# Kernel tuning notes

Hardware: AMD Instinct MI355X
Metric: run time of the kernel (lower is better)

Reference implementation:

```python
import jax, jax.numpy as jnp
import numpy as np

RANK_WEIGHT = 0.1  # init kwarg rank_weight
EPS = 1e-08


def setup_inputs() -> dict:
    key = jax.random.key(0)
    k1, k2, k3, k4 = jax.random.split(key, 4)
    B, D = 8192, 128
    return {
        "q_embeddings": jax.random.normal(k1, (B, D), dtype=jnp.float32),
        "a_embeddings": jax.random.normal(k2, (B, D), dtype=jnp.float32),
        "question_ids": jax.random.randint(k3, (B,), 0, 2048, dtype=jnp.int64),
        "ranks": jax.random.uniform(k4, (B,), dtype=jnp.float32),
    }


def reference(q_embeddings, a_embeddings, question_ids, ranks):
    # NOTE: the original computes q@a.T/temperature into `similarity` but the
    # per-sample loop recomputes sims WITHOUT temperature; we match the loop math.
    sims = jnp.matmul(q_embeddings, a_embeddings.T)  # [B, B]
    same_q = question_ids[:, None] == question_ids[None, :]  # [B, B] bool
    # pos_mask weight per positive column j: 1 - rank_weight * ranks[j]
    w = jnp.where(same_q, 1.0 - RANK_WEIGHT * ranks[None, :], 0.0)  # [B, B]
    # stable exp-ratio: sum(w*exp(s)) / sum(exp(s))
    m = jnp.max(sims, axis=1, keepdims=True)
    e = jnp.exp(sims - m)
    num = jnp.sum(w * e, axis=1)
    den = jnp.sum(e, axis=1)
    loss = jnp.mean(-jnp.log(num / den + EPS))
    pred = jnp.argmax(sims, axis=1)  # [B]
    correct = jnp.take_along_axis(w, pred[:, None], axis=1)[:, 0] > 0
    accuracy = jnp.mean(correct.astype(jnp.float32))
    return loss, accuracy
```

## Files before the change

### kernel.cpp

```cpp
#include <hip/hip_runtime.h>
#include <hip/hip_bf16.h>
#include <cmath>

#define B_N 8192
#define D_K 128
#define ROWS 64
#define CSPLIT 8
#define T_OUT 16

typedef short bf16x8 __attribute__((ext_vector_type(8)));
typedef unsigned short u16x8 __attribute__((ext_vector_type(8)));
typedef float f32x4  __attribute__((ext_vector_type(4)));

typedef __attribute__((address_space(3))) unsigned int as3_uint;
typedef __attribute__((address_space(1))) unsigned int as1_uint;

__device__ __forceinline__ void gl_lds16(const void* g, void* l) {
    __builtin_amdgcn_global_load_lds((const as1_uint*)(uintptr_t)g,
                                     (as3_uint*)(unsigned int)(uintptr_t)l,
                                     16, 0, 0);
}

__device__ inline unsigned short f2bf(float f) {
    unsigned u = __builtin_bit_cast(unsigned, f);
    u += 0x7fffu + ((u >> 16) & 1u);
    return (unsigned short)(u >> 16);
}

__global__ void cvt_kernel(const float* __restrict__ q, const float* __restrict__ a,
                           unsigned short* __restrict__ qb, unsigned short* __restrict__ ab,
                           float* __restrict__ out) {
    int g = blockIdx.x * blockDim.x + threadIdx.x;
    if (g < 2) out[g] = 0.0f;
    float4 q0 = reinterpret_cast<const float4*>(q)[g * 2];
    float4 q1 = reinterpret_cast<const float4*>(q)[g * 2 + 1];
    u16x8 oq;
    oq[0] = f2bf(q0.x); oq[1] = f2bf(q0.y); oq[2] = f2bf(q0.z); oq[3] = f2bf(q0.w);
    oq[4] = f2bf(q1.x); oq[5] = f2bf(q1.y); oq[6] = f2bf(q1.z); oq[7] = f2bf(q1.w);
    *reinterpret_cast<u16x8*>(qb + (size_t)g * 8) = oq;

    float4 a0 = reinterpret_cast<const float4*>(a)[g * 2];
    float4 a1 = reinterpret_cast<const float4*>(a)[g * 2 + 1];
    u16x8 oa;
    oa[0] = f2bf(a0.x); oa[1] = f2bf(a0.y); oa[2] = f2bf(a0.z); oa[3] = f2bf(a0.w);
    oa[4] = f2bf(a1.x); oa[5] = f2bf(a1.y); oa[6] = f2bf(a1.z); oa[7] = f2bf(a1.w);
    const int col = g >> 4, sq = g & 15, s = sq >> 2, quad = sq & 3;
    const int chunk = ((col >> 4) * 4 + s) * 64 + quad * 16 + (col & 15);
    *reinterpret_cast<u16x8*>(ab + (size_t)chunk * 8) = oa;
}

__launch_bounds__(256, 4)
__global__ void mpl_part_kernel(const unsigned short* __restrict__ qb,
                                const unsigned short* __restrict__ ab,
                                const int* __restrict__ qids,
                                const float* __restrict__ ranks,
                                float* __restrict__ pden, float* __restrict__ pnum,
                                float* __restrict__ pmax, float* __restrict__ pmaxp) {
    __shared__ unsigned short smem[2 * 8192];

    const int tid  = threadIdx.x;
    const int lane = tid & 63;
    const int wave = tid >> 6;
    const int rg   = blockIdx.x >> 3;
    const int cs   = blockIdx.x & 7;
    const int rowBase = rg * ROWS;
    const int quad = lane >> 4;
    const int l15  = lane & 15;

    bf16x8 qfrag[4];
    {
        const unsigned short* qrow = qb + (size_t)(rowBase + wave * 16 + l15) * D_K + quad * 8;
        #pragma unroll
        for (int s = 0; s < 4; ++s)
            qfrag[s] = *reinterpret_cast<const bf16x8*>(qrow + s * 32);
    }

    int qidrow[4];
    #pragma unroll
    for (int r = 0; r < 4; ++r)
        qidrow[r] = qids[rowBase + wave * 16 + quad * 4 + r];

    float den[4], num[4], mxv[4], mxp[4];
    #pragma unroll
    for (int r = 0; r < 4; ++r) {
        den[r] = 0.f; num[r] = 0.f; mxv[r] = -INFINITY; mxp[r] = -INFINITY;
    }

    const float L2E = 1.4426950408889634f;
    const float CB  = 64.0f;
    const int colStart = cs * 1024;

    const char* gstrip = (const char*)ab + (size_t)cs * 64 * 4096;
    const int   chunk  = (wave * 4) * 1024;

    #pragma unroll
    for (int r = 0; r < 4; ++r)
        gl_lds16(gstrip + chunk + r * 1024 + lane * 16,
                 (char*)smem + chunk + r * 1024);
    __syncthreads();

    for (int t = 0; t < T_OUT; ++t) {
        const int cur = t & 1, nxt = cur ^ 1;
        if (t + 1 < T_OUT) {
            const char* gsrc = gstrip + (size_t)(t + 1) * 16384 + chunk;
            char*       ldst = (char*)smem + nxt * 16384 + chunk;
            #pragma unroll
            for (int r = 0; r < 4; ++r)
                gl_lds16(gsrc + r * 1024 + lane * 16, ldst + r * 1024);
        }

        const unsigned short* lbase = smem + cur * 8192 + lane * 8;
        f32x4 acc[4];
        #pragma unroll
        for (int u = 0; u < 4; ++u) acc[u] = f32x4{0.f, 0.f, 0.f, 0.f};
        #pragma unroll
        for (int u = 0; u < 4; ++u)
            #pragma unroll
            for (int s = 0; s < 4; ++s) {
                bf16x8 bfrag = *reinterpret_cast<const bf16x8*>(lbase + u * 2048 + s * 512);
                acc[u] = __builtin_amdgcn_mfma_f32_16x16x32_bf16(qfrag[s], bfrag, acc[u], 0, 0, 0);
            }

        #pragma unroll
        for (int u = 0; u < 4; ++u) {
            const int c  = colStart + t * 64 + u * 16 + l15;
            const int qc = qids[c];
            const float wc = 1.0f - 0.1f * ranks[c];
            #pragma unroll
            for (int r = 0; r < 4; ++r) {
                float sv = acc[u][r];
                float e  = __builtin_amdgcn_exp2f(fmaf(sv, L2E, -CB));
                bool pos = (qc == qidrow[r]);
                den[r] += e;
                num[r] = fmaf(pos ? wc : 0.0f, e, num[r]);
                mxv[r] = fmaxf(mxv[r], sv);
                mxp[r] = fmaxf(mxp[r], pos ? sv : -INFINITY);
            }
        }
        __syncthreads();
    }

    #pragma unroll
    for (int m = 1; m <= 8; m <<= 1) {
        #pragma unroll
        for (int r = 0; r < 4; ++r) {
            den[r] += __shfl_xor(den[r], m, 64);
            num[r] += __shfl_xor(num[r], m, 64);
            mxv[r]  = fmaxf(mxv[r], __shfl_xor(mxv[r], m, 64));
            mxp[r]  = fmaxf(mxp[r], __shfl_xor(mxp[r], m, 64));
        }
    }

    if (l15 == 0) {
        const int rb = cs * B_N + rowBase + wave * 16 + quad * 4;
        #pragma unroll
        for (int r = 0; r < 4; ++r) {
            pden[rb + r]  = den[r];
            pnum[rb + r]  = num[r];
            pmax[rb + r]  = mxv[r];
            pmaxp[rb + r] = mxp[r];
        }
    }
}

__launch_bounds__(256, 4)
__global__ void fin_kernel(const float* __restrict__ pden, const float* __restrict__ pnum,
                           const float* __restrict__ pmax, const float* __restrict__ pmaxp,
                           float* __restrict__ out) {
    const int r = blockIdx.x * 256 + threadIdx.x;
    float d = 0.f, n = 0.f, mv = -INFINITY, mp = -INFINITY;
    #pragma unroll
    for (int cs = 0; cs < CSPLIT; ++cs) {
        d += pden[cs * B_N + r];
        n += pnum[cs * B_N + r];
        mv = fmaxf(mv, pmax[cs * B_N + r]);
        mp = fmaxf(mp, pmaxp[cs * B_N + r]);
    }
    float lsum = -logf(n / d + 1e-8f);
    float csum = (mp == mv) ? 1.0f : 0.0f;
    #pragma unroll
    for (int m = 1; m <= 32; m <<= 1) {
        lsum += __shfl_xor(lsum, m, 64);
        csum += __shfl_xor(csum, m, 64);
    }
    __shared__ float sl[4], sc[4];
    const int wave = threadIdx.x >> 6;
    if ((threadIdx.x & 63) == 0) { sl[wave] = lsum; sc[wave] = csum; }
    __syncthreads();
    if (threadIdx.x == 0) {
        float L = sl[0] + sl[1] + sl[2] + sl[3];
        float C = sc[0] + sc[1] + sc[2] + sc[3];
        atomicAdd(&out[0], L * (1.0f / B_N));
        atomicAdd(&out[1], C * (1.0f / B_N));
    }
}

extern "C" void kernel_launch(void* const* d_in, const int* in_sizes, int n_in,
                              void* d_out, int out_size, void* d_ws, size_t ws_size,
                              hipStream_t stream) {
    const float* q     = (const float*)d_in[0];
    const float* a     = (const float*)d_in[1];
    const int*   qids  = (const int*)d_in[2];
    const float* ranks = (const float*)d_in[3];
    float* out = (float*)d_out;

    unsigned short* qb = (unsigned short*)d_ws;
    unsigned short* ab = qb + (size_t)B_N * D_K;
    char* p = (char*)(ab + (size_t)B_N * D_K);
    float* pden  = (float*)p;                p += CSPLIT * B_N * sizeof(float);
    float* pnum  = (float*)p;                p += CSPLIT * B_N * sizeof(float);
    float* pmax  = (float*)p;                p += CSPLIT * B_N * sizeof(float);
    float* pmaxp = (float*)p;

    cvt_kernel<<<(B_N * D_K / 8) / 256, 256, 0, stream>>>(q, a, qb, ab, out);
    mpl_part_kernel<<<(B_N / ROWS) * CSPLIT, 256, 0, stream>>>(qb, ab, qids, ranks,
                                                               pden, pnum, pmax, pmaxp);
    fin_kernel<<<B_N / 256, 256, 0, stream>>>(pden, pnum, pmax, pmaxp, out);
}
```

Measured before the change: 99.82 us.

## Switch to 32x32x16 MFMA tiles with 256-row, 512-thread blocks

Replaces the 16x16x32 bf16 MFMA with the 32x32x16 variant, so each wave computes a 32x32 tile. The A-matrix pre-layout is rewritten to match the new B-fragment lane mapping. Blocks now cover 256 rows with 8 waves (512 threads), so each LDS-staged column tile is reused by four times as many rows, cutting global/LDS traffic per MFMA. In exchange, per-thread accumulator and reduction state grows to 16 rows, which raises register pressure and halves blocks per CU. The grid shrinks to 256 blocks, which may underfill the GPU.

```diff
diff --git a/kernel.cpp b/kernel.cpp
--- a/kernel.cpp
+++ b/kernel.cpp
@@ -4,13 +4,13 @@
 
 #define B_N 8192
 #define D_K 128
-#define ROWS 64
+#define ROWS 256
 #define CSPLIT 8
 #define T_OUT 16
 
 typedef short bf16x8 __attribute__((ext_vector_type(8)));
 typedef unsigned short u16x8 __attribute__((ext_vector_type(8)));
-typedef float f32x4  __attribute__((ext_vector_type(4)));
+typedef float f32x16 __attribute__((ext_vector_type(16)));
 
 typedef __attribute__((address_space(3))) unsigned int as3_uint;
 typedef __attribute__((address_space(1))) unsigned int as1_uint;
@@ -44,12 +44,14 @@
     u16x8 oa;
     oa[0] = f2bf(a0.x); oa[1] = f2bf(a0.y); oa[2] = f2bf(a0.z); oa[3] = f2bf(a0.w);
     oa[4] = f2bf(a1.x); oa[5] = f2bf(a1.y); oa[6] = f2bf(a1.z); oa[7] = f2bf(a1.w);
-    const int col = g >> 4, sq = g & 15, s = sq >> 2, quad = sq & 3;
-    const int chunk = ((col >> 4) * 4 + s) * 64 + quad * 16 + (col & 15);
-    *reinterpret_cast<u16x8*>(ab + (size_t)chunk * 8) = oa;
-}
-
-__launch_bounds__(256, 4)
+    const int col = g >> 4, sq = g & 15;
+    const int N = col >> 5, nl = col & 31;
+    const int s16 = sq >> 1, h = sq & 1;
+    const int lane = h * 32 + nl;
+    *reinterpret_cast<u16x8*>(ab + (size_t)(N * 8 + s16) * 512 + lane * 8) = oa;
+}
+
+__launch_bounds__(512, 2)
 __global__ void mpl_part_kernel(const unsigned short* __restrict__ qb,
                                 const unsigned short* __restrict__ ab,
                                 const int* __restrict__ qids,
@@ -63,26 +65,26 @@
     const int wave = tid >> 6;
     const int rg   = blockIdx.x >> 3;
     const int cs   = blockIdx.x & 7;
-    const int rowBase = rg * ROWS;
-    const int quad = lane >> 4;
-    const int l15  = lane & 15;
-
-    bf16x8 qfrag[4];
+    const int waveRow = rg * ROWS + wave * 32;
+    const int half = lane >> 5;
+    const int l31  = lane & 31;
+
+    bf16x8 qfrag[8];
     {
-        const unsigned short* qrow = qb + (size_t)(rowBase + wave * 16 + l15) * D_K + quad * 8;
-        #pragma unroll
-        for (int s = 0; s < 4; ++s)
-            qfrag[s] = *reinterpret_cast<const bf16x8*>(qrow + s * 32);
-    }
-
-    int qidrow[4];
-    #pragma unroll
-    for (int r = 0; r < 4; ++r)
-        qidrow[r] = qids[rowBase + wave * 16 + quad * 4 + r];
-
-    float den[4], num[4], mxv[4], mxp[4];
-    #pragma unroll
-    for (int r = 0; r < 4; ++r) {
+        const unsigned short* qrow = qb + (size_t)(waveRow + l31) * D_K + half * 8;
+        #pragma unroll
+        for (int s = 0; s < 8; ++s)
+            qfrag[s] = *reinterpret_cast<const bf16x8*>(qrow + s * 16);
+    }
+
+    int qidrow[16];
+    #pragma unroll
+    for (int r = 0; r < 16; ++r)
+        qidrow[r] = qids[waveRow + (r & 3) + 8 * (r >> 2) + 4 * half];
+
+    float den[16], num[16], mxv[16], mxp[16];
+    #pragma unroll
+    for (int r = 0; r < 16; ++r) {
         den[r] = 0.f; num[r] = 0.f; mxv[r] = -INFINITY; mxp[r] = -INFINITY;
     }
 
@@ -90,13 +92,13 @@
     const float CB  = 64.0f;
     const int colStart = cs * 1024;
 
-    const char* gstrip = (const char*)ab + (size_t)cs * 64 * 4096;
-    const int   chunk  = (wave * 4) * 1024;
-
-    #pragma unroll
-    for (int r = 0; r < 4; ++r)
-        gl_lds16(gstrip + chunk + r * 1024 + lane * 16,
-                 (char*)smem + chunk + r * 1024);
+    const char* gstrip = (const char*)ab + (size_t)cs * 262144;
+    const int   chunk  = wave * 2048;
+
+    #pragma unroll
+    for (int i = 0; i < 2; ++i)
+        gl_lds16(gstrip + chunk + i * 1024 + lane * 16,
+                 (char*)smem + chunk + i * 1024);
     __syncthreads();
 
     for (int t = 0; t < T_OUT; ++t) {
@@ -105,30 +107,29 @@
             const char* gsrc = gstrip + (size_t)(t + 1) * 16384 + chunk;
             char*       ldst = (char*)smem + nxt * 16384 + chunk;
             #pragma unroll
-            for (int r = 0; r < 4; ++r)
-                gl_lds16(gsrc + r * 1024 + lane * 16, ldst + r * 1024);
+            for (int i = 0; i < 2; ++i)
+                gl_lds16(gsrc + i * 1024 + lane * 16, ldst + i * 1024);
         }
 
         const unsigned short* lbase = smem + cur * 8192 + lane * 8;
-        f32x4 acc[4];
-        #pragma unroll
-        for (int u = 0; u < 4; ++u) acc[u] = f32x4{0.f, 0.f, 0.f, 0.f};
-        #pragma unroll
-        for (int u = 0; u < 4; ++u)
-            #pragma unroll
-            for (int s = 0; s < 4; ++s) {
-                bf16x8 bfrag = *reinterpret_cast<const bf16x8*>(lbase + u * 2048 + s * 512);
-                acc[u] = __builtin_amdgcn_mfma_f32_16x16x32_bf16(qfrag[s], bfrag, acc[u], 0, 0, 0);
-            }
-
-        #pragma unroll
-        for (int u = 0; u < 4; ++u) {
-            const int c  = colStart + t * 64 + u * 16 + l15;
+        #pragma unroll
+        for (int nt = 0; nt < 2; ++nt) {
+            const int c  = colStart + t * 64 + nt * 32 + l31;
             const int qc = qids[c];
             const float wc = 1.0f - 0.1f * ranks[c];
-            #pragma unroll
-            for (int r = 0; r < 4; ++r) {
-                float sv = acc[u][r];
+
+            f32x16 acc;
+            #pragma unroll
+            for (int i = 0; i < 16; ++i) acc[i] = 0.f;
+            #pragma unroll
+            for (int s = 0; s < 8; ++s) {
+                bf16x8 bfrag = *reinterpret_cast<const bf16x8*>(lbase + nt * 4096 + s * 512);
+                acc = __builtin_amdgcn_mfma_f32_32x32x16_bf16(qfrag[s], bfrag, acc, 0, 0, 0);
+            }
+
+            #pragma unroll
+            for (int r = 0; r < 16; ++r) {
+                float sv = acc[r];
                 float e  = __builtin_amdgcn_exp2f(fmaf(sv, L2E, -CB));
                 bool pos = (qc == qidrow[r]);
                 den[r] += e;
@@ -141,9 +142,9 @@
     }
 
     #pragma unroll
-    for (int m = 1; m <= 8; m <<= 1) {
-        #pragma unroll
-        for (int r = 0; r < 4; ++r) {
+    for (int m = 1; m <= 16; m <<= 1) {
+        #pragma unroll
+        for (int r = 0; r < 16; ++r) {
             den[r] += __shfl_xor(den[r], m, 64);
             num[r] += __shfl_xor(num[r], m, 64);
             mxv[r]  = fmaxf(mxv[r], __shfl_xor(mxv[r], m, 64));
@@ -151,14 +152,14 @@
         }
     }
 
-    if (l15 == 0) {
-        const int rb = cs * B_N + rowBase + wave * 16 + quad * 4;
-        #pragma unroll
-        for (int r = 0; r < 4; ++r) {
-            pden[rb + r]  = den[r];
-            pnum[rb + r]  = num[r];
-            pmax[rb + r]  = mxv[r];
-            pmaxp[rb + r] = mxp[r];
+    if (l31 == 0) {
+        #pragma unroll
+        for (int r = 0; r < 16; ++r) {
+            const int row = waveRow + (r & 3) + 8 * (r >> 2) + 4 * half;
+            pden[cs * B_N + row]  = den[r];
+            pnum[cs * B_N + row]  = num[r];
+            pmax[cs * B_N + row]  = mxv[r];
+            pmaxp[cs * B_N + row] = mxp[r];
         }
     }
 }
@@ -213,7 +214,7 @@
     float* pmaxp = (float*)p;
 
     cvt_kernel<<<(B_N * D_K / 8) / 256, 256, 0, stream>>>(q, a, qb, ab, out);
-    mpl_part_kernel<<<(B_N / ROWS) * CSPLIT, 256, 0, stream>>>(qb, ab, qids, ranks,
+    mpl_part_kernel<<<(B_N / ROWS) * CSPLIT, 512, 0, stream>>>(qb, ab, qids, ranks,
                                                                pden, pnum, pmax, pmaxp);
     fin_kernel<<<B_N / 256, 256, 0, stream>>>(pden, pnum, pmax, pmaxp, out);
 }
```

Result: slower. 104.9 us (+5.1%).

## Switch similarity GEMM from bf16 to fp8 MFMA with repacked LDS layout

Applied to the files above, without the earlier changes.

Embeddings are now converted to fp8 (e4m3) instead of bf16, and the similarity matmul uses the fp8 16x16x32 MFMA. The column-tile layout is repacked so each pipeline stage covers 128 columns in 16 KB of LDS, halving the loop trip count. The aim is to halve operand bandwidth and raise MFMA throughput. fp8 precision loss can change argmax ties and the accuracy metric, and it adds loss error that may exceed tolerance.

```diff
diff --git a/kernel.cpp b/kernel.cpp
--- a/kernel.cpp
+++ b/kernel.cpp
@@ -1,16 +1,14 @@
 #include <hip/hip_runtime.h>
-#include <hip/hip_bf16.h>
 #include <cmath>
 
 #define B_N 8192
 #define D_K 128
 #define ROWS 64
 #define CSPLIT 8
-#define T_OUT 16
-
-typedef short bf16x8 __attribute__((ext_vector_type(8)));
-typedef unsigned short u16x8 __attribute__((ext_vector_type(8)));
-typedef float f32x4  __attribute__((ext_vector_type(4)));
+#define T_OUT 8
+
+typedef float f32x4 __attribute__((ext_vector_type(4)));
+typedef long  lx2   __attribute__((ext_vector_type(2)));
 
 typedef __attribute__((address_space(3))) unsigned int as3_uint;
 typedef __attribute__((address_space(1))) unsigned int as1_uint;
@@ -21,42 +19,44 @@
                                      16, 0, 0);
 }
 
-__device__ inline unsigned short f2bf(float f) {
-    unsigned u = __builtin_bit_cast(unsigned, f);
-    u += 0x7fffu + ((u >> 16) & 1u);
-    return (unsigned short)(u >> 16);
-}
-
 __global__ void cvt_kernel(const float* __restrict__ q, const float* __restrict__ a,
-                           unsigned short* __restrict__ qb, unsigned short* __restrict__ ab,
+                           unsigned char* __restrict__ qp, unsigned char* __restrict__ ap,
                            float* __restrict__ out) {
-    int g = blockIdx.x * blockDim.x + threadIdx.x;
+    const int g = blockIdx.x * blockDim.x + threadIdx.x;
     if (g < 2) out[g] = 0.0f;
+
     float4 q0 = reinterpret_cast<const float4*>(q)[g * 2];
     float4 q1 = reinterpret_cast<const float4*>(q)[g * 2 + 1];
-    u16x8 oq;
-    oq[0] = f2bf(q0.x); oq[1] = f2bf(q0.y); oq[2] = f2bf(q0.z); oq[3] = f2bf(q0.w);
-    oq[4] = f2bf(q1.x); oq[5] = f2bf(q1.y); oq[6] = f2bf(q1.z); oq[7] = f2bf(q1.w);
-    *reinterpret_cast<u16x8*>(qb + (size_t)g * 8) = oq;
-
     float4 a0 = reinterpret_cast<const float4*>(a)[g * 2];
     float4 a1 = reinterpret_cast<const float4*>(a)[g * 2 + 1];
-    u16x8 oa;
-    oa[0] = f2bf(a0.x); oa[1] = f2bf(a0.y); oa[2] = f2bf(a0.z); oa[3] = f2bf(a0.w);
-    oa[4] = f2bf(a1.x); oa[5] = f2bf(a1.y); oa[6] = f2bf(a1.z); oa[7] = f2bf(a1.w);
-    const int col = g >> 4, sq = g & 15, s = sq >> 2, quad = sq & 3;
-    const int chunk = ((col >> 4) * 4 + s) * 64 + quad * 16 + (col & 15);
-    *reinterpret_cast<u16x8*>(ab + (size_t)chunk * 8) = oa;
+
+    int qw0 = __builtin_amdgcn_cvt_pk_fp8_f32(q0.x, q0.y, 0, false);
+    qw0     = __builtin_amdgcn_cvt_pk_fp8_f32(q0.z, q0.w, qw0, true);
+    int qw1 = __builtin_amdgcn_cvt_pk_fp8_f32(q1.x, q1.y, 0, false);
+    qw1     = __builtin_amdgcn_cvt_pk_fp8_f32(q1.z, q1.w, qw1, true);
+    int aw0 = __builtin_amdgcn_cvt_pk_fp8_f32(a0.x, a0.y, 0, false);
+    aw0     = __builtin_amdgcn_cvt_pk_fp8_f32(a0.z, a0.w, aw0, true);
+    int aw1 = __builtin_amdgcn_cvt_pk_fp8_f32(a1.x, a1.y, 0, false);
+    aw1     = __builtin_amdgcn_cvt_pk_fp8_f32(a1.z, a1.w, aw1, true);
+
+    *reinterpret_cast<int2*>(qp + (size_t)g * 8) = make_int2(qw0, qw1);
+
+    const int col = g >> 4, sq = g & 15;
+    const int s = sq >> 2, quad = sq & 3;
+    const int T = col >> 4, e = col & 15;
+    const size_t off = (size_t)T * 2048 + (size_t)(s >> 1) * 1024
+                     + (size_t)(quad * 16 + e) * 16 + (size_t)(s & 1) * 8;
+    *reinterpret_cast<int2*>(ap + off) = make_int2(aw0, aw1);
 }
 
 __launch_bounds__(256, 4)
-__global__ void mpl_part_kernel(const unsigned short* __restrict__ qb,
-                                const unsigned short* __restrict__ ab,
+__global__ void mpl_part_kernel(const unsigned char* __restrict__ qp,
+                                const unsigned char* __restrict__ ap,
                                 const int* __restrict__ qids,
                                 const float* __restrict__ ranks,
                                 float* __restrict__ pden, float* __restrict__ pnum,
                                 float* __restrict__ pmax, float* __restrict__ pmaxp) {
-    __shared__ unsigned short smem[2 * 8192];
+    __shared__ unsigned char smem[2 * 16384];
 
     const int tid  = threadIdx.x;
     const int lane = tid & 63;
@@ -67,12 +67,12 @@
     const int quad = lane >> 4;
     const int l15  = lane & 15;
 
-    bf16x8 qfrag[4];
+    long qfrag[4];
     {
-        const unsigned short* qrow = qb + (size_t)(rowBase + wave * 16 + l15) * D_K + quad * 8;
+        const unsigned char* qrow = qp + (size_t)(rowBase + wave * 16 + l15) * D_K + quad * 8;
         #pragma unroll
         for (int s = 0; s < 4; ++s)
-            qfrag[s] = *reinterpret_cast<const bf16x8*>(qrow + s * 32);
+            qfrag[s] = *reinterpret_cast<const long*>(qrow + s * 32);
     }
 
     int qidrow[4];
@@ -90,13 +90,13 @@
     const float CB  = 64.0f;
     const int colStart = cs * 1024;
 
-    const char* gstrip = (const char*)ab + (size_t)cs * 64 * 4096;
-    const int   chunk  = (wave * 4) * 1024;
-
-    #pragma unroll
-    for (int r = 0; r < 4; ++r)
-        gl_lds16(gstrip + chunk + r * 1024 + lane * 16,
-                 (char*)smem + chunk + r * 1024);
+    const char* gstrip = (const char*)ap + (size_t)cs * 131072;
+    const int   chunk  = wave * 4096;
+
+    #pragma unroll
+    for (int i = 0; i < 4; ++i)
+        gl_lds16(gstrip + chunk + i * 1024 + lane * 16,
+                 (char*)smem + chunk + i * 1024);
     __syncthreads();
 
     for (int t = 0; t < T_OUT; ++t) {
@@ -105,30 +105,28 @@
             const char* gsrc = gstrip + (size_t)(t + 1) * 16384 + chunk;
             char*       ldst = (char*)smem + nxt * 16384 + chunk;
             #pragma unroll
-            for (int r = 0; r < 4; ++r)
-                gl_lds16(gsrc + r * 1024 + lane * 16, ldst + r * 1024);
-        }
-
-        const unsigned short* lbase = smem + cur * 8192 + lane * 8;
-        f32x4 acc[4];
-        #pragma unroll
-        for (int u = 0; u < 4; ++u) acc[u] = f32x4{0.f, 0.f, 0.f, 0.f};
-        #pragma unroll
-        for (int u = 0; u < 4; ++u)
-            #pragma unroll
-            for (int s = 0; s < 4; ++s) {
-                bf16x8 bfrag = *reinterpret_cast<const bf16x8*>(lbase + u * 2048 + s * 512);
-                acc[u] = __builtin_amdgcn_mfma_f32_16x16x32_bf16(qfrag[s], bfrag, acc[u], 0, 0, 0);
-            }
-
-        #pragma unroll
-        for (int u = 0; u < 4; ++u) {
-            const int c  = colStart + t * 64 + u * 16 + l15;
+            for (int i = 0; i < 4; ++i)
+                gl_lds16(gsrc + i * 1024 + lane * 16, ldst + i * 1024);
+        }
+
+        const unsigned char* lbase = smem + cur * 16384 + lane * 16;
+        #pragma unroll
+        for (int u = 0; u < 8; ++u) {
+            lx2 b01 = *reinterpret_cast<const lx2*>(lbase + u * 2048);
+            lx2 b23 = *reinterpret_cast<const lx2*>(lbase + u * 2048 + 1024);
+
+            f32x4 acc = {0.f, 0.f, 0.f, 0.f};
+            acc = __builtin_amdgcn_mfma_f32_16x16x32_fp8_fp8(qfrag[0], b01[0], acc, 0, 0, 0);
+            acc = __builtin_amdgcn_mfma_f32_16x16x32_fp8_fp8(qfrag[1], b01[1], acc, 0, 0, 0);
+            acc = __builtin_amdgcn_mfma_f32_16x16x32_fp8_fp8(qfrag[2], b23[0], acc, 0, 0, 0);
+            acc = __builtin_amdgcn_mfma_f32_16x16x32_fp8_fp8(qfrag[3], b23[1], acc, 0, 0, 0);
+
+            const int c  = colStart + t * 128 + u * 16 + l15;
             const int qc = qids[c];
             const float wc = 1.0f - 0.1f * ranks[c];
             #pragma unroll
             for (int r = 0; r < 4; ++r) {
-                float sv = acc[u][r];
+                float sv = acc[r];
                 float e  = __builtin_amdgcn_exp2f(fmaf(sv, L2E, -CB));
                 bool pos = (qc == qidrow[r]);
                 den[r] += e;
@@ -204,16 +202,16 @@
     const float* ranks = (const float*)d_in[3];
     float* out = (float*)d_out;
 
-    unsigned short* qb = (unsigned short*)d_ws;
-    unsigned short* ab = qb + (size_t)B_N * D_K;
-    char* p = (char*)(ab + (size_t)B_N * D_K);
+    unsigned char* qp = (unsigned char*)d_ws;
+    unsigned char* ap = qp + (size_t)B_N * D_K;
+    char* p = (char*)(ap + (size_t)B_N * D_K);
     float* pden  = (float*)p;                p += CSPLIT * B_N * sizeof(float);
     float* pnum  = (float*)p;                p += CSPLIT * B_N * sizeof(float);
     float* pmax  = (float*)p;                p += CSPLIT * B_N * sizeof(float);
     float* pmaxp = (float*)p;
 
-    cvt_kernel<<<(B_N * D_K / 8) / 256, 256, 0, stream>>>(q, a, qb, ab, out);
-    mpl_part_kernel<<<(B_N / ROWS) * CSPLIT, 256, 0, stream>>>(qb, ab, qids, ranks,
+    cvt_kernel<<<(B_N * D_K / 8) / 256, 256, 0, stream>>>(q, a, qp, ap, out);
+    mpl_part_kernel<<<(B_N / ROWS) * CSPLIT, 256, 0, stream>>>(qp, ap, qids, ranks,
                                                                pden, pnum, pmax, pmaxp);
     fin_kernel<<<B_N / 256, 256, 0, stream>>>(pden, pnum, pmax, pmaxp, out);
 }
```

Result: faster. 95.32 us (median of 2 runs) (-4.5%).
